# Performance work log

Measured on AMD Instinct MI355X. Metric: run time of the kernel, lower is better.

The kernel has to match this reference:

```python
import jax, jax.numpy as jnp
import numpy as np

B = 64          # graphs per batch
NN = 4096       # nodes per graph (64x64 lattice)
N = B * NN      # total nodes
DEG = 4         # avg degree
E = N * DEG     # total directed edges
DIN, H, L = 1, 128, 64


def setup_inputs() -> dict:
    key = jax.random.key(0)
    ks = jax.random.split(key, 16)
    x = jax.random.normal(ks[0], (N, DIN), dtype=jnp.float32)
    eps = jax.random.normal(ks[1], (B, L), dtype=jnp.float32)
    # per-graph random edges, offset so they never cross graphs
    src = jax.random.randint(ks[2], (E,), 0, NN)
    dst = jax.random.randint(ks[3], (E,), 0, NN)
    off = (jnp.arange(E) // (NN * DEG)) * NN
    edge_index = jnp.stack([src + off, dst + off]).astype(jnp.int32)
    batch = (jnp.arange(N) // NN).astype(jnp.int32)
    s = 0.02
    p = lambda k, shp: s * jax.random.normal(k, shp, dtype=jnp.float32)
    return {
        "x": x, "eps": eps,
        "enc_w1": p(ks[4], (DIN, H)), "enc_b1": jnp.zeros((H,), jnp.float32),
        "enc_w2": p(ks[5], (H, H)),   "enc_b2": jnp.zeros((H,), jnp.float32),
        "mu_w": p(ks[6], (H, L)),     "mu_b": jnp.zeros((L,), jnp.float32),
        "lv_w": p(ks[7], (H, L)),     "lv_b": jnp.zeros((L,), jnp.float32),
        "zn_w": p(ks[8], (L, H)),     "zn_b": jnp.zeros((H,), jnp.float32),
        "dec_w1": p(ks[9], (H, H)),   "dec_b1": jnp.zeros((H,), jnp.float32),
        "dec_w2": p(ks[10], (H, H)),  "dec_b2": jnp.zeros((H,), jnp.float32),
        "out_w": p(ks[11], (H, 1)),   "out_b": jnp.zeros((1,), jnp.float32),
        "edge_index": edge_index, "batch": batch,
    }


def _gcn(h, w, b, row, col, norm, n):
    # PyG GCNConv: xW -> gather at row, scale by sym-norm, scatter-sum at col, + bias
    hw = h @ w
    msg = hw[row] * norm[:, None]
    return jax.ops.segment_sum(msg, col, num_segments=n) + b


def reference(x, eps, enc_w1, enc_b1, enc_w2, enc_b2, mu_w, mu_b, lv_w, lv_b,
              zn_w, zn_b, dec_w1, dec_b1, dec_w2, dec_b2, out_w, out_b,
              edge_index, batch):
    n = x.shape[0]
    b = eps.shape[0]
    nn_ = n // b
    # add self-loops, symmetric GCN normalization (shared by all convs)
    loops = jnp.arange(n, dtype=edge_index.dtype)
    row = jnp.concatenate([edge_index[0], loops])
    col = jnp.concatenate([edge_index[1], loops])
    deg = jax.ops.segment_sum(jnp.ones_like(col, dtype=x.dtype), col, num_segments=n)
    dinv = jnp.where(deg > 0, jax.lax.rsqrt(deg), 0.0)
    norm = dinv[row] * dinv[col]
    h = jax.nn.relu(_gcn(x, enc_w1, enc_b1, row, col, norm, n))
    h = jax.nn.relu(_gcn(h, enc_w2, enc_b2, row, col, norm, n))
    cnt = jax.ops.segment_sum(jnp.ones((n,), x.dtype), batch, num_segments=b)
    hg = jax.ops.segment_sum(h, batch, num_segments=b) / cnt[:, None]
    mu = hg @ mu_w + mu_b
    logvar = hg @ lv_w + lv_b
    # ---- reparameterize ----
    z = mu + jnp.exp(0.5 * logvar) * eps
    zn = z @ zn_w + zn_b          # [B, H]
    hd = zn[batch]                # [N, H]
    hd = jax.nn.relu(_gcn(hd, dec_w1, dec_b1, row, col, norm, n))
    hd = jax.nn.relu(_gcn(hd, dec_w2, dec_b2, row, col, norm, n))
    spin = jnp.tanh(hd @ out_w + out_b)   # [N, 1]
    recon = spin.reshape(b, nn_)
    return (recon, mu, logvar, z)
```

## Files before the change

kernel.cpp:

```cpp
#include <hip/hip_runtime.h>
#include <math.h>

#define NTOT 262144
#define BG   64
#define NNPG 4096
#define ET   1048576
#define EPG  16384
#define EPB  4096
#define HD   128
#define LD   64
#define NSEG 129
#define TN   256
#define MCAP ET

__device__ __forceinline__ void swz(int b, int& g, int& j){
  int xcd = b & 7, q = b >> 3;
  g = (q >> 2)*8 + xcd;
  j = q & 3;
}

__device__ __forceinline__ void tabrows_body(
    int g, int tid,
    const float* __restrict__ wsrc, const float* __restrict__ bsrc,
    const float* __restrict__ w2, const int* __restrict__ segUsed,
    const int* __restrict__ nfA, float* __restrict__ ACbase,
    float* ws, float* bs, float* tsh, int* ks, int* rr,
    float (*red)[128][4])
{
  int k = tid & 127, qg = tid >> 7;
  if (qg == 0){
    float w = wsrc[g*HD + k], b = bsrc[k];
    float t; int kind;
    if (w != 0.0f){ t = -b / w; kind = (w > 0.0f) ? 0 : 1; }
    else          { t = INFINITY; kind = 2; }
    ws[k] = w; bs[k] = b; tsh[k] = t; ks[k] = kind;
  }
  __syncthreads();
  if (qg == 0){
    float t = tsh[k];
    int r = 0;
    for (int q = 0; q < 128; q++){
      if (ks[q] != 2){
        float tq = tsh[q];
        if (tq < t || (tq == t && q < k)) r++;
      }
    }
    rr[k] = r;
  }
  float a0=0.f, c0=0.f, an=0.f, cn=0.f;
  #pragma unroll
  for (int u = 0; u < 16; u++){
    int q = qg*16 + u;
    float v = w2[q*HD + k];
    int kd = ks[q];
    float wq = ws[q], bq = bs[q];
    bool m0 = (kd == 1) || (kd == 2 && bq > 0.f);
    bool mn = (kd == 0) || (kd == 2 && bq > 0.f);
    float wv = wq*v, bv = bq*v;
    a0 += m0 ? wv : 0.f; c0 += m0 ? bv : 0.f;
    an += mn ? wv : 0.f; cn += mn ? bv : 0.f;
  }
  red[qg][k][0]=a0; red[qg][k][1]=c0; red[qg][k][2]=an; red[qg][k][3]=cn;
  __syncthreads();
  int nf = nfA[g];
  float* ACg = ACbase + (size_t)g*NSEG*256;
  int base = (k>>2)*8 + (k&3);
  if (qg == 0){
    float A0=0.f,C0=0.f,An=0.f,Cn=0.f;
    #pragma unroll
    for (int p = 0; p < 8; p++){
      A0+=red[p][k][0]; C0+=red[p][k][1]; An+=red[p][k][2]; Cn+=red[p][k][3];
    }
    ACg[base] = A0; ACg[base+4] = C0;
    ACg[(size_t)nf*256 + base] = An; ACg[(size_t)nf*256 + base + 4] = Cn;
  }
  __syncthreads();
  for (int wd = 0; wd < 5; wd++){
    unsigned m = (unsigned)segUsed[g*8 + wd];
    if (wd == 0) m &= ~1u;
    if ((nf >> 5) == wd) m &= ~(1u << (nf & 31));
    while (m){
      int bit = __ffs(m) - 1;
      m &= m - 1;
      int s = wd*32 + bit;
      float pa=0.f, pc=0.f;
      #pragma unroll
      for (int u = 0; u < 16; u++){
        int q = qg*16 + u;
        int kd = ks[q];
        bool act = (kd == 0) ? (rr[q] < s) : (kd == 1) ? (rr[q] >= s) : (bs[q] > 0.f);
        float v = act ? w2[q*HD + k] : 0.f;
        pa = fmaf(ws[q], v, pa); pc = fmaf(bs[q], v, pc);
      }
      red[qg][k][0]=pa; red[qg][k][1]=pc;
      __syncthreads();
      if (qg == 0){
        float A=0.f,C=0.f;
        #pragma unroll
        for (int p = 0; p < 8; p++){ A+=red[p][k][0]; C+=red[p][k][1]; }
        ACg[(size_t)s*256 + base] = A; ACg[(size_t)s*256 + base + 4] = C;
      }
      __syncthreads();
    }
  }
}

__global__ void __launch_bounds__(1024) k_count(const int* __restrict__ ei,
                                                const float* __restrict__ w1,
                                                const float* __restrict__ b1,
                                                int* __restrict__ cntJ,
                                                float* __restrict__ t1, int* __restrict__ nfp,
                                                float* __restrict__ hgsum,
                                                int* __restrict__ mcnt,
                                                int* __restrict__ segU1,
                                                int* __restrict__ segU){
  __shared__ int h[NNPG];
  int tid = threadIdx.x;
  if (blockIdx.x == 256){
    for (int idx = tid; idx < BG*HD; idx += 1024) hgsum[idx] = 0.f;
    if (tid < 2) mcnt[tid] = 0;
    if (tid < 8) segU1[tid] = 0;
    if (tid < BG*8) segU[tid] = 0;
    if (tid < 128){
      float w = w1[tid], b = b1[tid];
      float t; int kind;
      if (w != 0.0f){ t = -b / w; kind = (w > 0.0f) ? 0 : 1; }
      else          { t = INFINITY; kind = 2; }
      h[tid] = kind;
      t1[tid] = t;
    }
    __syncthreads();
    if (tid == 0){
      int c = 0;
      for (int q = 0; q < 128; q++) c += (h[q] != 2) ? 1 : 0;
      nfp[0] = c;
    }
    return;
  }
  int g, j; swz(blockIdx.x, g, j);
  #pragma unroll
  for (int k = tid; k < NNPG; k += 1024) h[k] = 0;
  __syncthreads();
  int gbase = g*NNPG;
  const int4* dsts4 = (const int4*)(ei + ET + g*EPG + j*EPB);
  int4 D = dsts4[tid];
  atomicAdd(&h[D.x - gbase], 1); atomicAdd(&h[D.y - gbase], 1);
  atomicAdd(&h[D.z - gbase], 1); atomicAdd(&h[D.w - gbase], 1);
  __syncthreads();
  int* plane = cntJ + j*NTOT + gbase;
  #pragma unroll
  for (int k = tid; k < NNPG; k += 1024) plane[k] = h[k];
}

__global__ void __launch_bounds__(1024) k_edge1(
    const int* __restrict__ ei, const int* __restrict__ cntJ,
    const float* __restrict__ x, float2* __restrict__ xd,
    float2* __restrict__ accJ)
{
  __shared__ float2 sxd[NNPG];
  __shared__ float ax[NNPG];
  __shared__ float s1[NNPG];
  int tid = threadIdx.x;
  int g, j; swz(blockIdx.x, g, j);
  int gbase = g*NNPG;
  const int4* srcs4 = (const int4*)(ei + g*EPG + j*EPB);
  const int4* dsts4 = (const int4*)(ei + ET + g*EPG + j*EPB);
  int4 S = srcs4[tid], D = dsts4[tid];
  {
    int i0 = 4*tid;
    int4 c0 = *(const int4*)(cntJ + 0*NTOT + gbase + i0);
    int4 c1 = *(const int4*)(cntJ + 1*NTOT + gbase + i0);
    int4 c2 = *(const int4*)(cntJ + 2*NTOT + gbase + i0);
    int4 c3 = *(const int4*)(cntJ + 3*NTOT + gbase + i0);
    float4 xv = *(const float4*)(x + gbase + i0);
    float2 p0 = make_float2(xv.x, rsqrtf((float)(c0.x+c1.x+c2.x+c3.x) + 1.0f));
    float2 p1 = make_float2(xv.y, rsqrtf((float)(c0.y+c1.y+c2.y+c3.y) + 1.0f));
    float2 p2 = make_float2(xv.z, rsqrtf((float)(c0.z+c1.z+c2.z+c3.z) + 1.0f));
    float2 p3 = make_float2(xv.w, rsqrtf((float)(c0.w+c1.w+c2.w+c3.w) + 1.0f));
    sxd[i0+0] = p0; sxd[i0+1] = p1; sxd[i0+2] = p2; sxd[i0+3] = p3;
    if (j == 0){
      float4* xd4 = (float4*)(xd + gbase);
      xd4[2*tid+0] = make_float4(p0.x, p0.y, p1.x, p1.y);
      xd4[2*tid+1] = make_float4(p2.x, p2.y, p3.x, p3.y);
    }
    *(float4*)(ax + i0) = make_float4(0.f,0.f,0.f,0.f);
    *(float4*)(s1 + i0) = make_float4(0.f,0.f,0.f,0.f);
  }
  __syncthreads();
  #define P1(s_, d_) { float2 sd = sxd[(s_) - gbase]; int dl = (d_) - gbase; \
    atomicAdd(&ax[dl], sd.y * sd.x); \
    atomicAdd(&s1[dl], sd.y); }
  P1(S.x, D.x); P1(S.y, D.y); P1(S.z, D.z); P1(S.w, D.w);
  #undef P1
  __syncthreads();
  float4* ap = (float4*)(accJ + (size_t)j*NTOT + gbase);
  ap[2*tid+0] = make_float4(ax[4*tid+0], s1[4*tid+0], ax[4*tid+1], s1[4*tid+1]);
  ap[2*tid+1] = make_float4(ax[4*tid+2], s1[4*tid+2], ax[4*tid+3], s1[4*tid+3]);
}

__global__ void k_pack(const float2* __restrict__ xd, const float2* __restrict__ accJ,
                       const float* __restrict__ t1,
                       float4* __restrict__ rec, float* __restrict__ srowA,
                       int* __restrict__ segU1){
  __shared__ float ts[128];
  __shared__ int used[8];
  int tid = threadIdx.x;
  if (tid < 128) ts[tid] = t1[tid];
  if (tid < 8) used[tid] = 0;
  __syncthreads();
  int i = blockIdx.x*256 + tid;
  float2 xdv = xd[i];
  float2 a0 = accJ[0*NTOT + i], a1 = accJ[1*NTOT + i];
  float2 a2 = accJ[2*NTOT + i], a3 = accJ[3*NTOT + i];
  float axs = (a0.x + a1.x) + (a2.x + a3.x);
  float s1s = (a0.y + a1.y) + (a2.y + a3.y);
  float di = xdv.y;
  float ax = di * (di * xdv.x + axs);
  float sr = di * (di + s1s);
  int sc = 0;
  for (int q = 0; q < 128; q++) sc += (ts[q] < ax) ? 1 : 0;
  rec[i] = make_float4(di, di*ax, di*sr, __int_as_float(sc));
  srowA[i] = sr;
  atomicOr(&used[sc>>5], 1u << (sc & 31));
  __syncthreads();
  if (tid < 8 && used[tid]) atomicOr(&segU1[tid], used[tid]);
}

__global__ void __launch_bounds__(1024) k_edge2enc(
    const int* __restrict__ ei, const float4* __restrict__ rec,
    const int* __restrict__ nfp, float4* __restrict__ sums4,
    int2* __restrict__ missL, int* __restrict__ mcnt,
    const float* __restrict__ enc_w1, const float* __restrict__ enc_b1,
    const float* __restrict__ enc_w2, const int* __restrict__ segU1,
    float* __restrict__ AC1)
{
  __shared__ union {
    struct { float sf[NNPG*4]; float4 sRec[NNPG]; } e;
    struct { float ws[128], bs[128], tsh[128];
             int ks[128], rr[128]; float red[8][128][4]; } t;
  } u;
  int tid = threadIdx.x;
  if (blockIdx.x == 256){
    tabrows_body(0, tid, enc_w1, enc_b1, enc_w2, segU1, nfp, AC1,
                 u.t.ws, u.t.bs, u.t.tsh, u.t.ks, u.t.rr, u.t.red);
    return;
  }
  int g, j; swz(blockIdx.x, g, j);
  int gbase = g*NNPG;
  int nf = nfp[0];
  const int4* srcs4 = (const int4*)(ei + g*EPG + j*EPB);
  const int4* dsts4 = (const int4*)(ei + ET + g*EPG + j*EPB);
  int4 S = srcs4[tid], D = dsts4[tid];
  float4* sf4 = (float4*)u.e.sf;
  #pragma unroll
  for (int k = 0; k < 4; k++){
    sf4[4*tid + k] = make_float4(0.f,0.f,0.f,0.f);
    u.e.sRec[k*1024 + tid] = rec[gbase + k*1024 + tid];
  }
  __syncthreads();
  #define E1(s_, d_) { float4 r = u.e.sRec[(s_) - gbase]; int dl = (d_) - gbase; \
    int sb = __float_as_int(r.w); \
    atomicAdd(&u.e.sf[dl*4+0], r.y); atomicAdd(&u.e.sf[dl*4+1], r.x); \
    if (sb == nf) { atomicAdd(&u.e.sf[dl*4+2], r.y); atomicAdd(&u.e.sf[dl*4+3], r.x); } \
    else if (sb != 0) { int ix = atomicAdd(&mcnt[0], 1); \
      if (ix < MCAP) missL[ix] = make_int2(d_, s_); } }
  E1(S.x, D.x); E1(S.y, D.y); E1(S.z, D.z); E1(S.w, D.w);
  #undef E1
  __syncthreads();
  float4* sp = sums4 + (size_t)j*NTOT + gbase;
  #pragma unroll
  for (int k = 0; k < 4; k++) sp[4*tid + k] = sf4[4*tid + k];
}

__global__ void __launch_bounds__(256) k_enc_fin(
    const float4* __restrict__ rec, const float4* __restrict__ sums4,
    const float4* __restrict__ AC, const float* __restrict__ b2,
    const int* __restrict__ nfp, const int2* __restrict__ missL,
    const int* __restrict__ mcnt, float* __restrict__ hgsum)
{
  __shared__ float4 sS[TN];
  __shared__ float4 sRA[TN];
  __shared__ float red[256*4];
  int bid = blockIdx.x, g = bid & 63, part = bid >> 6;
  int tid = threadIdx.x, lane = tid & 31, nrow = tid >> 5;
  int base = g*NNPG + part*TN;
  int nf = nfp[0];
  {
    int i = base + tid;
    sRA[tid] = rec[i];
    float4 a = sums4[0*NTOT + i], b = sums4[1*NTOT + i];
    float4 c = sums4[2*NTOT + i], d = sums4[3*NTOT + i];
    sS[tid] = make_float4(a.x+b.x+c.x+d.x, a.y+b.y+c.y+d.y,
                          a.z+b.z+c.z+d.z, a.w+b.w+c.w+d.w);
  }
  __syncthreads();
  const float4* q0 = AC + (size_t)lane*2;
  const float4* qn = AC + ((size_t)nf*32 + lane)*2;
  float4 A0 = q0[0], C0 = q0[1], An = qn[0], Cn = qn[1];
  float4 dA = make_float4(An.x-A0.x, An.y-A0.y, An.z-A0.z, An.w-A0.w);
  float4 dC = make_float4(Cn.x-C0.x, Cn.y-C0.y, Cn.z-C0.z, Cn.w-C0.w);
  float4 bb = ((const float4*)b2)[lane];
  int mc = mcnt[0]; mc = mc < MCAP ? mc : MCAP;
  float gx=0.f, gy=0.f, gz=0.f, gw=0.f;
  for (int it = 0; it < TN/8; ++it){
    int li = it*8 + nrow;
    int i = base + li;
    float4 rA = sRA[li];
    float4 s4 = sS[li];
    float accx = fmaf(s4.x,A0.x, fmaf(s4.z,dA.x, fmaf(s4.y,C0.x, s4.w*dC.x)));
    float accy = fmaf(s4.x,A0.y, fmaf(s4.z,dA.y, fmaf(s4.y,C0.y, s4.w*dC.y)));
    float accz = fmaf(s4.x,A0.z, fmaf(s4.z,dA.z, fmaf(s4.y,C0.z, s4.w*dC.z)));
    float accw = fmaf(s4.x,A0.w, fmaf(s4.z,dA.w, fmaf(s4.y,C0.w, s4.w*dC.w)));
    if (mc > 0){
      for (int e = 0; e < mc; e++){
        int2 me = missL[e];
        if (me.x == i){
          float4 r = rec[me.y];
          int sb = __float_as_int(r.w);
          const float4* qm = AC + ((size_t)sb*32 + lane)*2;
          float4 qa = qm[0], qc = qm[1];
          accx = fmaf(r.y, qa.x-A0.x, fmaf(r.x, qc.x-C0.x, accx));
          accy = fmaf(r.y, qa.y-A0.y, fmaf(r.x, qc.y-C0.y, accy));
          accz = fmaf(r.y, qa.z-A0.z, fmaf(r.x, qc.z-C0.z, accz));
          accw = fmaf(r.y, qa.w-A0.w, fmaf(r.x, qc.w-C0.w, accw));
        }
      }
    }
    int si = __float_as_int(rA.w);
    bool m0 = (si == 0);
    float4 sa, sc;
    sa.x = m0 ? A0.x : An.x; sa.y = m0 ? A0.y : An.y; sa.z = m0 ? A0.z : An.z; sa.w = m0 ? A0.w : An.w;
    sc.x = m0 ? C0.x : Cn.x; sc.y = m0 ? C0.y : Cn.y; sc.z = m0 ? C0.z : Cn.z; sc.w = m0 ? C0.w : Cn.w;
    if (si != 0 && si != nf){
      const float4* qs = AC + ((size_t)si*32 + lane)*2;
      sa = qs[0]; sc = qs[1];
    }
    float d = rA.x, d2 = d*d, ca = rA.y*d;
    gx += fmaxf(fmaf(d, accx, fmaf(ca, sa.x, d2*sc.x)) + bb.x, 0.f);
    gy += fmaxf(fmaf(d, accy, fmaf(ca, sa.y, d2*sc.y)) + bb.y, 0.f);
    gz += fmaxf(fmaf(d, accz, fmaf(ca, sa.z, d2*sc.z)) + bb.z, 0.f);
    gw += fmaxf(fmaf(d, accw, fmaf(ca, sa.w, d2*sc.w)) + bb.w, 0.f);
  }
  __syncthreads();
  red[tid*4+0] = gx; red[tid*4+1] = gy; red[tid*4+2] = gz; red[tid*4+3] = gw;
  __syncthreads();
  if (nrow == 0){
    float tx=0.f, ty=0.f, tz=0.f, tw=0.f;
    for (int r2 = 0; r2 < 8; r2++){
      int t2 = (r2*32 + lane)*4;
      tx += red[t2]; ty += red[t2+1]; tz += red[t2+2]; tw += red[t2+3];
    }
    atomicAdd(&hgsum[g*HD + lane*4 + 0], tx);
    atomicAdd(&hgsum[g*HD + lane*4 + 1], ty);
    atomicAdd(&hgsum[g*HD + lane*4 + 2], tz);
    atomicAdd(&hgsum[g*HD + lane*4 + 3], tw);
  }
}

__global__ void __launch_bounds__(128) k_small(
    const float* __restrict__ hgsum,
    const float* __restrict__ mu_w, const float* __restrict__ mu_b,
    const float* __restrict__ lv_w, const float* __restrict__ lv_b,
    const float* __restrict__ eps,
    const float* __restrict__ zn_w, const float* __restrict__ zn_b,
    const float* __restrict__ dec_w1, const float* __restrict__ dec_b1,
    float* __restrict__ out_mu, float* __restrict__ out_lv, float* __restrict__ out_z,
    float* __restrict__ t2, float* __restrict__ ushG, int* __restrict__ nf2)
{
  int g = blockIdx.x, tid = threadIdx.x;
  __shared__ float hg[128], zsh[64], znsh[128];
  __shared__ int ks[128];
  hg[tid] = hgsum[g*HD + tid] * (1.0f/4096.0f);
  __syncthreads();
  if (tid < 64){
    int l = tid;
    float m = mu_b[l], v = lv_b[l];
    for (int k = 0; k < HD; k++){
      float hv = hg[k];
      m = fmaf(hv, mu_w[k*LD + l], m);
      v = fmaf(hv, lv_w[k*LD + l], v);
    }
    int o = g*LD + l;
    out_mu[o] = m; out_lv[o] = v;
    float zv = fmaf(expf(0.5f*v), eps[o], m);
    out_z[o] = zv; zsh[l] = zv;
  }
  __syncthreads();
  {
    int k = tid;
    float acc = zn_b[k];
    for (int l = 0; l < LD; l++) acc = fmaf(zsh[l], zn_w[l*HD + k], acc);
    znsh[k] = acc;
  }
  __syncthreads();
  float w;
  {
    int k = tid;
    float acc = 0.f;
    for (int j = 0; j < HD; j++) acc = fmaf(znsh[j], dec_w1[j*HD + k], acc);
    ushG[g*HD + k] = acc;
    w = acc;
  }
  float b = dec_b1[tid];
  float t; int kind;
  if (w != 0.0f){ t = -b / w; kind = (w > 0.0f) ? 0 : 1; }
  else          { t = INFINITY; kind = 2; }
  t2[g*HD + tid] = t; ks[tid] = kind;
  __syncthreads();
  if (tid == 0){
    int c = 0;
    for (int q = 0; q < 128; q++) c += (ks[q] != 2) ? 1 : 0;
    nf2[g] = c;
  }
}

__global__ void k_seg2(const float* __restrict__ t2, const float* __restrict__ srowA,
                       float4* __restrict__ rec, int* __restrict__ segUsed){
  __shared__ float ts[128];
  __shared__ int used[8];
  int tid = threadIdx.x;
  int i = blockIdx.x*256 + tid;
  int g = blockIdx.x >> 4;
  if (tid < 128) ts[tid] = t2[g*HD + tid];
  if (tid < 8) used[tid] = 0;
  __syncthreads();
  float a = srowA[i];
  int sc = 0;
  for (int q = 0; q < 128; q++) sc += (ts[q] < a) ? 1 : 0;
  float4 r = rec[i];
  r.y = __int_as_float(sc);
  rec[i] = r;
  atomicOr(&used[sc>>5], 1u << (sc & 31));
  __syncthreads();
  if (tid < 8 && used[tid]) atomicOr(&segUsed[g*8 + tid], used[tid]);
}

__global__ void __launch_bounds__(1024) k_edge2dec(
    const int* __restrict__ ei, const float4* __restrict__ rec,
    const int* __restrict__ nf2, float4* __restrict__ sums4,
    int2* __restrict__ missL, int* __restrict__ mcnt,
    const float* __restrict__ ushG, const float* __restrict__ dec_b1,
    const float* __restrict__ dec_w2, const int* __restrict__ segU,
    float* __restrict__ AC2)
{
  __shared__ union {
    struct { float sf[NNPG*4]; float4 sRec[NNPG]; } e;
    struct { float ws[128], bs[128], tsh[128];
             int ks[128], rr[128]; float red[8][128][4]; } t;
  } u;
  int tid = threadIdx.x;
  if (blockIdx.x >= 256){
    tabrows_body(blockIdx.x - 256, tid, ushG, dec_b1, dec_w2, segU, nf2, AC2,
                 u.t.ws, u.t.bs, u.t.tsh, u.t.ks, u.t.rr, u.t.red);
    return;
  }
  int g, j; swz(blockIdx.x, g, j);
  int gbase = g*NNPG;
  int nf = nf2[g];
  const int4* srcs4 = (const int4*)(ei + g*EPG + j*EPB);
  const int4* dsts4 = (const int4*)(ei + ET + g*EPG + j*EPB);
  int4 S = srcs4[tid], D = dsts4[tid];
  float4* sf4 = (float4*)u.e.sf;
  #pragma unroll
  for (int k = 0; k < 4; k++){
    sf4[4*tid + k] = make_float4(0.f,0.f,0.f,0.f);
    u.e.sRec[k*1024 + tid] = rec[gbase + k*1024 + tid];
  }
  __syncthreads();
  #define E2(s_, d_) { float4 r = u.e.sRec[(s_) - gbase]; int dl = (d_) - gbase; \
    int sb = __float_as_int(r.y); \
    atomicAdd(&u.e.sf[dl*4+0], r.z); atomicAdd(&u.e.sf[dl*4+1], r.x); \
    if (sb == nf) { atomicAdd(&u.e.sf[dl*4+2], r.z); atomicAdd(&u.e.sf[dl*4+3], r.x); } \
    else if (sb != 0) { int ix = atomicAdd(&mcnt[1], 1); \
      if (ix < MCAP) missL[ix] = make_int2(d_, s_); } }
  E2(S.x, D.x); E2(S.y, D.y); E2(S.z, D.z); E2(S.w, D.w);
  #undef E2
  __syncthreads();
  float4* sp = sums4 + (size_t)j*NTOT + gbase;
  #pragma unroll
  for (int k = 0; k < 4; k++) sp[4*tid + k] = sf4[4*tid + k];
}

__global__ void __launch_bounds__(256) k_dec_fin(
    const float4* __restrict__ rec, const float4* __restrict__ sums4,
    const float4* __restrict__ AC2, const float* __restrict__ b2,
    const float* __restrict__ ow, const float* __restrict__ ob,
    const int* __restrict__ nf2, const int2* __restrict__ missL,
    const int* __restrict__ mcnt, float* __restrict__ recon)
{
  __shared__ float4 sS[TN];
  __shared__ float4 sRA[TN];
  int bid = blockIdx.x, g = bid & 63, part = bid >> 6;
  int tid = threadIdx.x, lane = tid & 31, nrow = tid >> 5;
  int base = g*NNPG + part*TN;
  int nf = nf2[g];
  const float4* AC = AC2 + (size_t)g*NSEG*64;
  {
    int i = base + tid;
    sRA[tid] = rec[i];
    float4 a = sums4[0*NTOT + i], b = sums4[1*NTOT + i];
    float4 c = sums4[2*NTOT + i], d = sums4[3*NTOT + i];
    sS[tid] = make_float4(a.x+b.x+c.x+d.x, a.y+b.y+c.y+d.y,
                          a.z+b.z+c.z+d.z, a.w+b.w+c.w+d.w);
  }
  __syncthreads();
  const float4* q0 = AC + (size_t)lane*2;
  const float4* qn = AC + ((size_t)nf*32 + lane)*2;
  float4 A0 = q0[0], C0 = q0[1], An = qn[0], Cn = qn[1];
  float4 dA = make_float4(An.x-A0.x, An.y-A0.y, An.z-A0.z, An.w-A0.w);
  float4 dC = make_float4(Cn.x-C0.x, Cn.y-C0.y, Cn.z-C0.z, Cn.w-C0.w);
  float4 bb  = ((const float4*)b2)[lane];
  float4 owv = ((const float4*)ow)[lane];
  float obv = ob[0];
  int mc = mcnt[1]; mc = mc < MCAP ? mc : MCAP;
  for (int it = 0; it < TN/8; ++it){
    int li = it*8 + nrow;
    int i = base + li;
    float4 rA = sRA[li];
    float4 s4 = sS[li];
    float accx = fmaf(s4.x,A0.x, fmaf(s4.z,dA.x, fmaf(s4.y,C0.x, s4.w*dC.x)));
    float accy = fmaf(s4.x,A0.y, fmaf(s4.z,dA.y, fmaf(s4.y,C0.y, s4.w*dC.y)));
    float accz = fmaf(s4.x,A0.z, fmaf(s4.z,dA.z, fmaf(s4.y,C0.z, s4.w*dC.z)));
    float accw = fmaf(s4.x,A0.w, fmaf(s4.z,dA.w, fmaf(s4.y,C0.w, s4.w*dC.w)));
    if (mc > 0){
      for (int e = 0; e < mc; e++){
        int2 me = missL[e];
        if (me.x == i){
          float4 r = rec[me.y];
          int sb = __float_as_int(r.y);
          const float4* qm = AC + ((size_t)sb*32 + lane)*2;
          float4 qa = qm[0], qc = qm[1];
          accx = fmaf(r.z, qa.x-A0.x, fmaf(r.x, qc.x-C0.x, accx));
          accy = fmaf(r.z, qa.y-A0.y, fmaf(r.x, qc.y-C0.y, accy));
          accz = fmaf(r.z, qa.z-A0.z, fmaf(r.x, qc.z-C0.z, accz));
          accw = fmaf(r.z, qa.w-A0.w, fmaf(r.x, qc.w-C0.w, accw));
        }
      }
    }
    int si = __float_as_int(rA.y);
    bool m0 = (si == 0);
    float4 sa, sc;
    sa.x = m0 ? A0.x : An.x; sa.y = m0 ? A0.y : An.y; sa.z = m0 ? A0.z : An.z; sa.w = m0 ? A0.w : An.w;
    sc.x = m0 ? C0.x : Cn.x; sc.y = m0 ? C0.y : Cn.y; sc.z = m0 ? C0.z : Cn.z; sc.w = m0 ? C0.w : Cn.w;
    if (si != 0 && si != nf){
      const float4* qs = AC + ((size_t)si*32 + lane)*2;
      sa = qs[0]; sc = qs[1];
    }
    float d = rA.x, d2 = d*d, ca = rA.z*d;
    float hx = fmaxf(fmaf(d, accx, fmaf(ca, sa.x, d2*sc.x)) + bb.x, 0.f);
    float hy = fmaxf(fmaf(d, accy, fmaf(ca, sa.y, d2*sc.y)) + bb.y, 0.f);
    float hz = fmaxf(fmaf(d, accz, fmaf(ca, sa.z, d2*sc.z)) + bb.z, 0.f);
    float hw = fmaxf(fmaf(d, accw, fmaf(ca, sa.w, d2*sc.w)) + bb.w, 0.f);
    float dsum = hx*owv.x + hy*owv.y + hz*owv.z + hw*owv.w;
    for (int o2 = 16; o2 > 0; o2 >>= 1) dsum += __shfl_down(dsum, o2, 32);
    if (lane == 0) recon[i] = tanhf(dsum + obv);
  }
}

extern "C" void kernel_launch(void* const* d_in, const int* in_sizes, int n_in,
                              void* d_out, int out_size, void* d_ws, size_t ws_size,
                              hipStream_t stream){
  (void)in_sizes; (void)n_in; (void)out_size; (void)ws_size;
  const float* x      = (const float*)d_in[0];
  const float* eps    = (const float*)d_in[1];
  const float* enc_w1 = (const float*)d_in[2];
  const float* enc_b1 = (const float*)d_in[3];
  const float* enc_w2 = (const float*)d_in[4];
  const float* enc_b2 = (const float*)d_in[5];
  const float* mu_w   = (const float*)d_in[6];
  const float* mu_b   = (const float*)d_in[7];
  const float* lv_w   = (const float*)d_in[8];
  const float* lv_b   = (const float*)d_in[9];
  const float* zn_w   = (const float*)d_in[10];
  const float* zn_b   = (const float*)d_in[11];
  const float* dec_w1 = (const float*)d_in[12];
  const float* dec_b1 = (const float*)d_in[13];
  const float* dec_w2 = (const float*)d_in[14];
  const float* dec_b2 = (const float*)d_in[15];
  const float* out_w  = (const float*)d_in[16];
  const float* out_b  = (const float*)d_in[17];
  const int*   ei     = (const int*)d_in[18];

  float* out       = (float*)d_out;
  float* out_recon = out;
  float* out_mu    = out + NTOT;
  float* out_lv    = out_mu + BG*LD;
  float* out_z     = out_lv + BG*LD;

  char* w = (char*)d_ws;
  size_t off_b = 0;
  auto alloc = [&](size_t bytes)->void*{
    void* p = w + off_b;
    off_b += (bytes + 255) & ~(size_t)255;
    return p;
  };
  char*   regA   = (char*) alloc((size_t)4*NTOT*16);
  int*    cntJ   = (int*)   regA;
  float2* accJ   = (float2*)(regA + (size_t)4*NTOT*4);
  float4* sums4  = (float4*)regA;
  float2* xd     = (float2*)alloc((size_t)NTOT*8);
  float4* rec    = (float4*)alloc((size_t)NTOT*16);
  float*  srowA  = (float*) alloc((size_t)NTOT*4);
  int2*   missL  = (int2*)  alloc((size_t)MCAP*8);
  float*  t1     = (float*) alloc(128*4);
  int*    nf1    = (int*)   alloc(256);
  int*    nf2    = (int*)   alloc(BG*4);
  int*    segU1  = (int*)   alloc(8*4);
  int*    segU   = (int*)   alloc(BG*8*4);
  float*  t2     = (float*) alloc((size_t)BG*HD*4);
  float*  ushG   = (float*) alloc((size_t)BG*HD*4);
  float*  AC1    = (float*) alloc((size_t)NSEG*256*4);
  float*  AC2    = (float*) alloc((size_t)BG*NSEG*256*4);
  float*  hgsum  = (float*) alloc((size_t)BG*HD*4);
  int*    mcnt   = (int*)   alloc(256);


  k_count <<<257, 1024, 0, stream>>>(ei, enc_w1, enc_b1, cntJ, t1, nf1,
                                     hgsum, mcnt, segU1, segU);
  k_edge1 <<<256, 1024, 0, stream>>>(ei, cntJ, x, xd, accJ);
  k_pack  <<<NTOT/256, 256, 0, stream>>>(xd, accJ, t1, rec, srowA, segU1);

  k_edge2enc<<<257, 1024, 0, stream>>>(ei, rec, nf1, sums4, missL, mcnt,
                                       enc_w1, enc_b1, enc_w2, segU1, AC1);
  k_enc_fin <<<1024, 256, 0, stream>>>(rec, sums4, (const float4*)AC1, enc_b2,
                                       nf1, missL, mcnt, hgsum);

  k_small<<<BG, 128, 0, stream>>>(hgsum, mu_w, mu_b, lv_w, lv_b, eps,
                                  zn_w, zn_b, dec_w1, dec_b1,
                                  out_mu, out_lv, out_z, t2, ushG, nf2);

  k_seg2<<<NTOT/256, 256, 0, stream>>>(t2, srowA, rec, segU);

  k_edge2dec<<<320, 1024, 0, stream>>>(ei, rec, nf2, sums4, missL, mcnt,
                                       ushG, dec_b1, dec_w2, segU, AC2);
  k_dec_fin <<<1024, 256, 0, stream>>>(rec, sums4, (const float4*)AC2, dec_b2,
                                       out_w, out_b, nf2, missL, mcnt, out_recon);
}
```

Before: 181.7 us.

## Hoist base table rows into earlier kernels and gather rec directly in edge passes

Splits the per-graph table construction into a base part (the all-off and all-on rows) and an extras part. The base part for the encoder now runs in the spare block of k_count, and for the decoder in a widened k_small (1024 threads), so the extra blocks in the edge kernels only run when intermediate segments are actually in use and can return early otherwise. The edge kernels no longer stage the whole per-graph rec array in shared memory; each thread gathers its four source records straight from global memory. This halves LDS use and removes a barrier-bound copy, at the cost of scattered global reads and a heavier k_small.

Measured after the change: 150.0 us (median of 2 runs). 1.21x faster.

```diff
diff --git a/kernel.cpp b/kernel.cpp
--- a/kernel.cpp
+++ b/kernel.cpp
@@ -19,33 +19,27 @@
   j = q & 3;
 }
 
-__device__ __forceinline__ void tabrows_body(
-    int g, int tid,
-    const float* __restrict__ wsrc, const float* __restrict__ bsrc,
-    const float* __restrict__ w2, const int* __restrict__ segUsed,
-    const int* __restrict__ nfA, float* __restrict__ ACbase,
-    float* ws, float* bs, float* tsh, int* ks, int* rr,
-    float (*red)[128][4])
+__device__ __forceinline__ void tab_base(
+    int tid, const float* __restrict__ wsrc, const float* __restrict__ bsrc,
+    const float* __restrict__ w2, float* __restrict__ tout, int* __restrict__ nfout,
+    float* __restrict__ ACg,
+    float* ws, float* bs, int* ks, float (*red)[128][4], int* nfsh)
 {
   int k = tid & 127, qg = tid >> 7;
   if (qg == 0){
-    float w = wsrc[g*HD + k], b = bsrc[k];
+    float w = wsrc[k], b = bsrc[k];
     float t; int kind;
     if (w != 0.0f){ t = -b / w; kind = (w > 0.0f) ? 0 : 1; }
     else          { t = INFINITY; kind = 2; }
-    ws[k] = w; bs[k] = b; tsh[k] = t; ks[k] = kind;
-  }
-  __syncthreads();
-  if (qg == 0){
-    float t = tsh[k];
-    int r = 0;
-    for (int q = 0; q < 128; q++){
-      if (ks[q] != 2){
-        float tq = tsh[q];
-        if (tq < t || (tq == t && q < k)) r++;
-      }
-    }
-    rr[k] = r;
+    ws[k] = w; bs[k] = b; ks[k] = kind;
+    if (tout) tout[k] = t;
+  }
+  __syncthreads();
+  if (tid == 0){
+    int c = 0;
+    for (int q = 0; q < 128; q++) c += (ks[q] != 2) ? 1 : 0;
+    *nfsh = c;
+    if (nfout) *nfout = c;
   }
   float a0=0.f, c0=0.f, an=0.f, cn=0.f;
   #pragma unroll
@@ -62,8 +56,7 @@
   }
   red[qg][k][0]=a0; red[qg][k][1]=c0; red[qg][k][2]=an; red[qg][k][3]=cn;
   __syncthreads();
-  int nf = nfA[g];
-  float* ACg = ACbase + (size_t)g*NSEG*256;
+  int nf = *nfsh;
   int base = (k>>2)*8 + (k&3);
   if (qg == 0){
     float A0=0.f,C0=0.f,An=0.f,Cn=0.f;
@@ -74,7 +67,46 @@
     ACg[base] = A0; ACg[base+4] = C0;
     ACg[(size_t)nf*256 + base] = An; ACg[(size_t)nf*256 + base + 4] = Cn;
   }
-  __syncthreads();
+}
+
+__device__ __forceinline__ void tab_extras(
+    int g, int tid, const float* __restrict__ wsrc, const float* __restrict__ bsrc,
+    const float* __restrict__ w2, const int* __restrict__ segUsed,
+    const int* __restrict__ nfA, float* __restrict__ ACbase,
+    float* ws, float* bs, float* tsh, int* ks, int* rr, float (*red)[128][4])
+{
+  int nf = nfA[g];
+  unsigned any = 0;
+  for (int wd = 0; wd < 5; wd++){
+    unsigned m = (unsigned)segUsed[g*8 + wd];
+    if (wd == 0) m &= ~1u;
+    if ((nf >> 5) == wd) m &= ~(1u << (nf & 31));
+    any |= m;
+  }
+  if (any == 0) return;
+  int k = tid & 127, qg = tid >> 7;
+  if (qg == 0){
+    float w = wsrc[g*HD + k], b = bsrc[k];
+    float t; int kind;
+    if (w != 0.0f){ t = -b / w; kind = (w > 0.0f) ? 0 : 1; }
+    else          { t = INFINITY; kind = 2; }
+    ws[k] = w; bs[k] = b; tsh[k] = t; ks[k] = kind;
+  }
+  __syncthreads();
+  if (qg == 0){
+    float t = tsh[k];
+    int r = 0;
+    for (int q = 0; q < 128; q++){
+      if (ks[q] != 2){
+        float tq = tsh[q];
+        if (tq < t || (tq == t && q < k)) r++;
+      }
+    }
+    rr[k] = r;
+  }
+  __syncthreads();
+  float* ACg = ACbase + (size_t)g*NSEG*256;
+  int base = (k>>2)*8 + (k&3);
   for (int wd = 0; wd < 5; wd++){
     unsigned m = (unsigned)segUsed[g*8 + wd];
     if (wd == 0) m &= ~1u;
@@ -108,48 +140,42 @@
 __global__ void __launch_bounds__(1024) k_count(const int* __restrict__ ei,
                                                 const float* __restrict__ w1,
                                                 const float* __restrict__ b1,
+                                                const float* __restrict__ w2,
                                                 int* __restrict__ cntJ,
                                                 float* __restrict__ t1, int* __restrict__ nfp,
+                                                float* __restrict__ AC1,
                                                 float* __restrict__ hgsum,
                                                 int* __restrict__ mcnt,
                                                 int* __restrict__ segU1,
                                                 int* __restrict__ segU){
-  __shared__ int h[NNPG];
+  __shared__ union {
+    int h[NNPG];
+    struct { float ws[128], bs[128]; int ks[128], nfsh;
+             float red[8][128][4]; } t;
+  } u;
   int tid = threadIdx.x;
   if (blockIdx.x == 256){
     for (int idx = tid; idx < BG*HD; idx += 1024) hgsum[idx] = 0.f;
     if (tid < 2) mcnt[tid] = 0;
     if (tid < 8) segU1[tid] = 0;
     if (tid < BG*8) segU[tid] = 0;
-    if (tid < 128){
-      float w = w1[tid], b = b1[tid];
-      float t; int kind;
-      if (w != 0.0f){ t = -b / w; kind = (w > 0.0f) ? 0 : 1; }
-      else          { t = INFINITY; kind = 2; }
-      h[tid] = kind;
-      t1[tid] = t;
-    }
-    __syncthreads();
-    if (tid == 0){
-      int c = 0;
-      for (int q = 0; q < 128; q++) c += (h[q] != 2) ? 1 : 0;
-      nfp[0] = c;
-    }
+    tab_base(tid, w1, b1, w2, t1, nfp, AC1,
+             u.t.ws, u.t.bs, u.t.ks, u.t.red, &u.t.nfsh);
     return;
   }
   int g, j; swz(blockIdx.x, g, j);
   #pragma unroll
-  for (int k = tid; k < NNPG; k += 1024) h[k] = 0;
+  for (int k = tid; k < NNPG; k += 1024) u.h[k] = 0;
   __syncthreads();
   int gbase = g*NNPG;
   const int4* dsts4 = (const int4*)(ei + ET + g*EPG + j*EPB);
   int4 D = dsts4[tid];
-  atomicAdd(&h[D.x - gbase], 1); atomicAdd(&h[D.y - gbase], 1);
-  atomicAdd(&h[D.z - gbase], 1); atomicAdd(&h[D.w - gbase], 1);
+  atomicAdd(&u.h[D.x - gbase], 1); atomicAdd(&u.h[D.y - gbase], 1);
+  atomicAdd(&u.h[D.z - gbase], 1); atomicAdd(&u.h[D.w - gbase], 1);
   __syncthreads();
   int* plane = cntJ + j*NTOT + gbase;
   #pragma unroll
-  for (int k = tid; k < NNPG; k += 1024) plane[k] = h[k];
+  for (int k = tid; k < NNPG; k += 1024) plane[k] = u.h[k];
 }
 
 __global__ void __launch_bounds__(1024) k_edge1(
@@ -235,14 +261,14 @@
     float* __restrict__ AC1)
 {
   __shared__ union {
-    struct { float sf[NNPG*4]; float4 sRec[NNPG]; } e;
+    float sf[NNPG*4];
     struct { float ws[128], bs[128], tsh[128];
              int ks[128], rr[128]; float red[8][128][4]; } t;
   } u;
   int tid = threadIdx.x;
   if (blockIdx.x == 256){
-    tabrows_body(0, tid, enc_w1, enc_b1, enc_w2, segU1, nfp, AC1,
-                 u.t.ws, u.t.bs, u.t.tsh, u.t.ks, u.t.rr, u.t.red);
+    tab_extras(0, tid, enc_w1, enc_b1, enc_w2, segU1, nfp, AC1,
+               u.t.ws, u.t.bs, u.t.tsh, u.t.ks, u.t.rr, u.t.red);
     return;
   }
   int g, j; swz(blockIdx.x, g, j);
@@ -251,25 +277,22 @@
   const int4* srcs4 = (const int4*)(ei + g*EPG + j*EPB);
   const int4* dsts4 = (const int4*)(ei + ET + g*EPG + j*EPB);
   int4 S = srcs4[tid], D = dsts4[tid];
-  float4* sf4 = (float4*)u.e.sf;
-  #pragma unroll
-  for (int k = 0; k < 4; k++){
-    sf4[4*tid + k] = make_float4(0.f,0.f,0.f,0.f);
-    u.e.sRec[k*1024 + tid] = rec[gbase + k*1024 + tid];
-  }
-  __syncthreads();
-  #define E1(s_, d_) { float4 r = u.e.sRec[(s_) - gbase]; int dl = (d_) - gbase; \
-    int sb = __float_as_int(r.w); \
-    atomicAdd(&u.e.sf[dl*4+0], r.y); atomicAdd(&u.e.sf[dl*4+1], r.x); \
-    if (sb == nf) { atomicAdd(&u.e.sf[dl*4+2], r.y); atomicAdd(&u.e.sf[dl*4+3], r.x); } \
+  float4 r1 = rec[S.x], r2 = rec[S.y], r3 = rec[S.z], r4 = rec[S.w];
+  float4* sf4 = (float4*)u.sf;
+  #pragma unroll
+  for (int k = 0; k < 4; k++) sf4[tid + k*1024] = make_float4(0.f,0.f,0.f,0.f);
+  __syncthreads();
+  #define E1(r_, s_, d_) { int dl = (d_) - gbase; int sb = __float_as_int(r_.w); \
+    atomicAdd(&u.sf[dl*4+0], r_.y); atomicAdd(&u.sf[dl*4+1], r_.x); \
+    if (sb == nf) { atomicAdd(&u.sf[dl*4+2], r_.y); atomicAdd(&u.sf[dl*4+3], r_.x); } \
     else if (sb != 0) { int ix = atomicAdd(&mcnt[0], 1); \
       if (ix < MCAP) missL[ix] = make_int2(d_, s_); } }
-  E1(S.x, D.x); E1(S.y, D.y); E1(S.z, D.z); E1(S.w, D.w);
+  E1(r1, S.x, D.x); E1(r2, S.y, D.y); E1(r3, S.z, D.z); E1(r4, S.w, D.w);
   #undef E1
   __syncthreads();
   float4* sp = sums4 + (size_t)j*NTOT + gbase;
   #pragma unroll
-  for (int k = 0; k < 4; k++) sp[4*tid + k] = sf4[4*tid + k];
+  for (int k = 0; k < 4; k++) sp[tid + k*1024] = sf4[tid + k*1024];
 }
 
 __global__ void __launch_bounds__(256) k_enc_fin(
@@ -357,20 +380,23 @@
   }
 }
 
-__global__ void __launch_bounds__(128) k_small(
+__global__ void __launch_bounds__(1024) k_small(
     const float* __restrict__ hgsum,
     const float* __restrict__ mu_w, const float* __restrict__ mu_b,
     const float* __restrict__ lv_w, const float* __restrict__ lv_b,
     const float* __restrict__ eps,
     const float* __restrict__ zn_w, const float* __restrict__ zn_b,
     const float* __restrict__ dec_w1, const float* __restrict__ dec_b1,
+    const float* __restrict__ dec_w2,
     float* __restrict__ out_mu, float* __restrict__ out_lv, float* __restrict__ out_z,
-    float* __restrict__ t2, float* __restrict__ ushG, int* __restrict__ nf2)
-{
+    float* __restrict__ t2, float* __restrict__ ushG, int* __restrict__ nf2,
+    float* __restrict__ AC2)
+{
+  __shared__ float hg[128], zsh[64], znsh[128], ush[128], bsx[128];
+  __shared__ int ks[128], nfsh;
+  __shared__ float red[8][128][4];
   int g = blockIdx.x, tid = threadIdx.x;
-  __shared__ float hg[128], zsh[64], znsh[128];
-  __shared__ int ks[128];
-  hg[tid] = hgsum[g*HD + tid] * (1.0f/4096.0f);
+  if (tid < 128) hg[tid] = hgsum[g*HD + tid] * (1.0f/4096.0f);
   __syncthreads();
   if (tid < 64){
     int l = tid;
@@ -386,31 +412,58 @@
     out_z[o] = zv; zsh[l] = zv;
   }
   __syncthreads();
-  {
-    int k = tid;
-    float acc = zn_b[k];
-    for (int l = 0; l < LD; l++) acc = fmaf(zsh[l], zn_w[l*HD + k], acc);
-    znsh[k] = acc;
-  }
-  __syncthreads();
-  float w;
-  {
-    int k = tid;
+  if (tid < 128){
+    float acc = zn_b[tid];
+    for (int l = 0; l < LD; l++) acc = fmaf(zsh[l], zn_w[l*HD + tid], acc);
+    znsh[tid] = acc;
+  }
+  __syncthreads();
+  if (tid < 128){
     float acc = 0.f;
-    for (int j = 0; j < HD; j++) acc = fmaf(znsh[j], dec_w1[j*HD + k], acc);
-    ushG[g*HD + k] = acc;
-    w = acc;
-  }
-  float b = dec_b1[tid];
-  float t; int kind;
-  if (w != 0.0f){ t = -b / w; kind = (w > 0.0f) ? 0 : 1; }
-  else          { t = INFINITY; kind = 2; }
-  t2[g*HD + tid] = t; ks[tid] = kind;
+    for (int j = 0; j < HD; j++) acc = fmaf(znsh[j], dec_w1[j*HD + tid], acc);
+    ushG[g*HD + tid] = acc;
+    ush[tid] = acc;
+    float b = dec_b1[tid];
+    bsx[tid] = b;
+    float t; int kind;
+    if (acc != 0.0f){ t = -b / acc; kind = (acc > 0.0f) ? 0 : 1; }
+    else            { t = INFINITY; kind = 2; }
+    t2[g*HD + tid] = t; ks[tid] = kind;
+  }
   __syncthreads();
   if (tid == 0){
     int c = 0;
     for (int q = 0; q < 128; q++) c += (ks[q] != 2) ? 1 : 0;
-    nf2[g] = c;
+    nf2[g] = c; nfsh = c;
+  }
+  __syncthreads();
+  int k = tid & 127, qg = tid >> 7;
+  float a0=0.f, c0=0.f, an=0.f, cn=0.f;
+  #pragma unroll
+  for (int u = 0; u < 16; u++){
+    int q = qg*16 + u;
+    float v = dec_w2[q*HD + k];
+    int kd = ks[q];
+    float wq = ush[q], bq = bsx[q];
+    bool m0 = (kd == 1) || (kd == 2 && bq > 0.f);
+    bool mn = (kd == 0) || (kd == 2 && bq > 0.f);
+    float wv = wq*v, bv = bq*v;
+    a0 += m0 ? wv : 0.f; c0 += m0 ? bv : 0.f;
+    an += mn ? wv : 0.f; cn += mn ? bv : 0.f;
+  }
+  red[qg][k][0]=a0; red[qg][k][1]=c0; red[qg][k][2]=an; red[qg][k][3]=cn;
+  __syncthreads();
+  if (qg == 0){
+    float A0=0.f,C0=0.f,An=0.f,Cn=0.f;
+    #pragma unroll
+    for (int p = 0; p < 8; p++){
+      A0+=red[p][k][0]; C0+=red[p][k][1]; An+=red[p][k][2]; Cn+=red[p][k][3];
+    }
+    float* ACg = AC2 + (size_t)g*NSEG*256;
+    int base = (k>>2)*8 + (k&3);
+    int nf = nfsh;
+    ACg[base] = A0; ACg[base+4] = C0;
+    ACg[(size_t)nf*256 + base] = An; ACg[(size_t)nf*256 + base + 4] = Cn;
   }
 }
 
@@ -444,14 +497,14 @@
     float* __restrict__ AC2)
 {
   __shared__ union {
-    struct { float sf[NNPG*4]; float4 sRec[NNPG]; } e;
+    float sf[NNPG*4];
     struct { float ws[128], bs[128], tsh[128];
              int ks[128], rr[128]; float red[8][128][4]; } t;
   } u;
   int tid = threadIdx.x;
   if (blockIdx.x >= 256){
-    tabrows_body(blockIdx.x - 256, tid, ushG, dec_b1, dec_w2, segU, nf2, AC2,
-                 u.t.ws, u.t.bs, u.t.tsh, u.t.ks, u.t.rr, u.t.red);
+    tab_extras(blockIdx.x - 256, tid, ushG, dec_b1, dec_w2, segU, nf2, AC2,
+               u.t.ws, u.t.bs, u.t.tsh, u.t.ks, u.t.rr, u.t.red);
     return;
   }
   int g, j; swz(blockIdx.x, g, j);
@@ -460,25 +513,22 @@
   const int4* srcs4 = (const int4*)(ei + g*EPG + j*EPB);
   const int4* dsts4 = (const int4*)(ei + ET + g*EPG + j*EPB);
   int4 S = srcs4[tid], D = dsts4[tid];
-  float4* sf4 = (float4*)u.e.sf;
-  #pragma unroll
-  for (int k = 0; k < 4; k++){
-    sf4[4*tid + k] = make_float4(0.f,0.f,0.f,0.f);
-    u.e.sRec[k*1024 + tid] = rec[gbase + k*1024 + tid];
-  }
-  __syncthreads();
-  #define E2(s_, d_) { float4 r = u.e.sRec[(s_) - gbase]; int dl = (d_) - gbase; \
-    int sb = __float_as_int(r.y); \
-    atomicAdd(&u.e.sf[dl*4+0], r.z); atomicAdd(&u.e.sf[dl*4+1], r.x); \
-    if (sb == nf) { atomicAdd(&u.e.sf[dl*4+2], r.z); atomicAdd(&u.e.sf[dl*4+3], r.x); } \
+  float4 r1 = rec[S.x], r2 = rec[S.y], r3 = rec[S.z], r4 = rec[S.w];
+  float4* sf4 = (float4*)u.sf;
+  #pragma unroll
+  for (int k = 0; k < 4; k++) sf4[tid + k*1024] = make_float4(0.f,0.f,0.f,0.f);
+  __syncthreads();
+  #define E2(r_, s_, d_) { int dl = (d_) - gbase; int sb = __float_as_int(r_.y); \
+    atomicAdd(&u.sf[dl*4+0], r_.z); atomicAdd(&u.sf[dl*4+1], r_.x); \
+    if (sb == nf) { atomicAdd(&u.sf[dl*4+2], r_.z); atomicAdd(&u.sf[dl*4+3], r_.x); } \
     else if (sb != 0) { int ix = atomicAdd(&mcnt[1], 1); \
       if (ix < MCAP) missL[ix] = make_int2(d_, s_); } }
-  E2(S.x, D.x); E2(S.y, D.y); E2(S.z, D.z); E2(S.w, D.w);
+  E2(r1, S.x, D.x); E2(r2, S.y, D.y); E2(r3, S.z, D.z); E2(r4, S.w, D.w);
   #undef E2
   __syncthreads();
   float4* sp = sums4 + (size_t)j*NTOT + gbase;
   #pragma unroll
-  for (int k = 0; k < 4; k++) sp[4*tid + k] = sf4[4*tid + k];
+  for (int k = 0; k < 4; k++) sp[tid + k*1024] = sf4[tid + k*1024];
 }
 
 __global__ void __launch_bounds__(256) k_dec_fin(
@@ -615,8 +665,8 @@
   int*    mcnt   = (int*)   alloc(256);
 
 
-  k_count <<<257, 1024, 0, stream>>>(ei, enc_w1, enc_b1, cntJ, t1, nf1,
-                                     hgsum, mcnt, segU1, segU);
+  k_count <<<257, 1024, 0, stream>>>(ei, enc_w1, enc_b1, enc_w2, cntJ, t1, nf1,
+                                     AC1, hgsum, mcnt, segU1, segU);
   k_edge1 <<<256, 1024, 0, stream>>>(ei, cntJ, x, xd, accJ);
   k_pack  <<<NTOT/256, 256, 0, stream>>>(xd, accJ, t1, rec, srowA, segU1);
 
@@ -625,9 +675,9 @@
   k_enc_fin <<<1024, 256, 0, stream>>>(rec, sums4, (const float4*)AC1, enc_b2,
                                        nf1, missL, mcnt, hgsum);
 
-  k_small<<<BG, 128, 0, stream>>>(hgsum, mu_w, mu_b, lv_w, lv_b, eps,
-                                  zn_w, zn_b, dec_w1, dec_b1,
-                                  out_mu, out_lv, out_z, t2, ushG, nf2);
+  k_small<<<BG, 1024, 0, stream>>>(hgsum, mu_w, mu_b, lv_w, lv_b, eps,
+                                   zn_w, zn_b, dec_w1, dec_b1, dec_w2,
+                                   out_mu, out_lv, out_z, t2, ushG, nf2, AC2);
 
   k_seg2<<<NTOT/256, 256, 0, stream>>>(t2, srowA, rec, segU);
 
```
